# Kernel optimization log

Hardware: AMD Instinct MI355X
Metric: run time of the kernel (lower is better)

The kernel has to match this reference:

```python
import jax, jax.numpy as jnp
import numpy as np

N, E, F, ED, H, C, B = 50000, 200000, 768, 768, 256, 3, 4096


def setup_inputs() -> dict:
    key = jax.random.key(0)
    ks = jax.random.split(key, 20)
    s = 0.05  # init scale for params
    inp = {
        "x": jax.random.normal(ks[0], (N, F), jnp.float32),
        "edge_attr": jax.random.normal(ks[1], (E, ED), jnp.float32),
        # GATConv layer 1 (in=F, out=H, heads=1, edge_dim=ED)
        "W1": jax.random.normal(ks[2], (F, H), jnp.float32) * s,
        "as1": jax.random.normal(ks[3], (H,), jnp.float32) * s,
        "ad1": jax.random.normal(ks[4], (H,), jnp.float32) * s,
        "We1": jax.random.normal(ks[5], (ED, H), jnp.float32) * s,
        "ae1": jax.random.normal(ks[6], (H,), jnp.float32) * s,
        "b1": jnp.zeros((H,), jnp.float32),
        # GATConv layer 2 (in=H, out=H)
        "W2": jax.random.normal(ks[7], (H, H), jnp.float32) * s,
        "as2": jax.random.normal(ks[8], (H,), jnp.float32) * s,
        "ad2": jax.random.normal(ks[9], (H,), jnp.float32) * s,
        "We2": jax.random.normal(ks[10], (ED, H), jnp.float32) * s,
        "ae2": jax.random.normal(ks[11], (H,), jnp.float32) * s,
        "b2": jnp.zeros((H,), jnp.float32),
        # prediction head
        "Wp": jax.random.normal(ks[12], (H, C), jnp.float32) * s,
        "bp": jnp.zeros((C,), jnp.float32),
        "edge_index": jax.random.randint(ks[13], (2, E), 0, N, jnp.int32),
        "nodes": jax.random.randint(ks[14], (2, B), 0, N, jnp.int32),
    }
    return inp


def gat_conv(x, edge_attr, src, dst, W, a_src, a_dst, We, a_e, b, n):
    # GATConv, heads=1, edge_dim attention, add_self_loops=False
    xl = x @ W  # [n, H]
    alpha_src = (xl * a_src).sum(-1)  # [n]
    alpha_dst = (xl * a_dst).sum(-1)  # [n]
    alpha_edge = ((edge_attr @ We) * a_e).sum(-1)  # [E]
    alpha = alpha_src[src] + alpha_dst[dst] + alpha_edge  # [E]
    alpha = jax.nn.leaky_relu(alpha, 0.2)
    # scatter-softmax over incoming edges of each destination node
    m = jax.ops.segment_max(alpha, dst, num_segments=n)
    e = jnp.exp(alpha - m[dst])
    den = jax.ops.segment_sum(e, dst, num_segments=n)
    coef = e / den[dst]  # [E]
    out = jax.ops.segment_sum(coef[:, None] * xl[src], dst, num_segments=n)
    return out + b


def reference(x, edge_attr, W1, as1, ad1, We1, ae1, b1, W2, as2, ad2, We2, ae2, b2, Wp, bp, edge_index, nodes):
    src, dst = edge_index[0], edge_index[1]
    n = x.shape[0]
    h = jax.nn.relu(gat_conv(x, edge_attr, src, dst, W1, as1, ad1, We1, ae1, b1, n))
    titles = gat_conv(h, edge_attr, src, dst, W2, as2, ad2, We2, ae2, b2, n)
    c = titles[nodes[0]] * titles[nodes[1]]  # [B, H]
    return c @ Wp + bp
```

## Files before the change

### kernel.cpp

```cpp
#include <hip/hip_runtime.h>
#include <math.h>

#define HDIM 256
#define FDIM 768
#define BM 128
#define BK 32

typedef __attribute__((ext_vector_type(8))) short short8;
typedef __attribute__((ext_vector_type(4))) float f32x4;
typedef __attribute__((ext_vector_type(4))) unsigned short us4;

__device__ __forceinline__ unsigned short f2bf(float f) {
  unsigned int u = __float_as_uint(f);
  unsigned int r = (u + 0x7FFFu + ((u >> 16) & 1u)) >> 16;
  return (unsigned short)r;
}
__device__ __forceinline__ float bf2f(unsigned short b) {
  return __uint_as_float(((unsigned int)b) << 16);
}

__device__ __forceinline__ void gload_lds16(const void* g, void* l) {
  __builtin_amdgcn_global_load_lds(
      (const __attribute__((address_space(1))) void*)g,
      (__attribute__((address_space(3))) void*)l, 16, 0, 0);
}


__device__ __forceinline__ void transpose_tile(const float* __restrict__ W,
                                               unsigned short* __restrict__ Wt,
                                               int K, int tk, int tn,
                                               float (*sT)[65], int t) {
  int lane = t & 63, rg = t >> 6;
  #pragma unroll
  for (int i = 0; i < 16; ++i) {
    int r = rg * 16 + i;
    sT[lane][r] = W[(size_t)(tk * 64 + r) * HDIM + tn * 64 + lane];
  }
  __syncthreads();
  #pragma unroll
  for (int i = 0; i < 16; ++i) {
    int h = rg * 16 + i;
    Wt[(size_t)(tn * 64 + h) * K + tk * 64 + lane] = f2bf(sT[h][lane]);
  }
}

__global__ __launch_bounds__(256) void k_prep(
    const float* __restrict__ We1, const float* __restrict__ ae1,
    const float* __restrict__ We2, const float* __restrict__ ae2,
    float* __restrict__ v1, float* __restrict__ v2,
    const float* __restrict__ W1, unsigned short* __restrict__ W1t,
    const float* __restrict__ W2, unsigned short* __restrict__ W2t,
    const int* __restrict__ dstArr, int* __restrict__ cnt, int E) {
  __shared__ float sT[64][65];
  int bid = blockIdx.x;
  int t = threadIdx.x;
  if (bid < 384) {
    int row = bid * 4 + (t >> 6);
    int lane = t & 63;
    const float* W = (row < FDIM) ? We1 : We2;
    const float* a = (row < FDIM) ? ae1 : ae2;
    int r = (row < FDIM) ? row : row - FDIM;
    float4 w = *(const float4*)&W[(size_t)r * HDIM + lane * 4];
    float4 av = *(const float4*)&a[lane * 4];
    float p = w.x * av.x + w.y * av.y + w.z * av.z + w.w * av.w;
    #pragma unroll
    for (int off = 32; off; off >>= 1) p += __shfl_down(p, off, 64);
    if (lane == 0) ((row < FDIM) ? v1 : v2)[r] = p;
  } else if (bid < 432) {
    int tile = bid - 384;
    transpose_tile(W1, W1t, FDIM, tile % 12, tile / 12, sT, t);
  } else if (bid < 448) {
    int tile = bid - 432;
    transpose_tile(W2, W2t, HDIM, tile & 3, tile >> 2, sT, t);
  } else {
    int e = (bid - 448) * 256 + t;
    if (e < E) atomicAdd(&cnt[dstArr[e]], 1);
  }
}


__global__ __launch_bounds__(256) void k_scan_lb(const int* __restrict__ cnt,
                                                 int* __restrict__ offsets,
                                                 int* __restrict__ cursor,
                                                 int* __restrict__ bsums,
                                                 int* __restrict__ flags, int n) {
  __shared__ int s[256];
  __shared__ int r[256];
  const int b = blockIdx.x, t = threadIdx.x;
  int i = b * 256 + t;
  int v = (i < n) ? cnt[i] : 0;
  s[t] = v;
  __syncthreads();
  for (int off = 1; off < 256; off <<= 1) {
    int tv = (t >= off) ? s[t - off] : 0;
    __syncthreads();
    s[t] += tv;
    __syncthreads();
  }
  if (t == 255) {
    bsums[b] = s[255];
    __threadfence();
    __hip_atomic_store(&flags[b], 1, __ATOMIC_RELEASE, __HIP_MEMORY_SCOPE_AGENT);
  }
  int contrib = 0;
  if (t < b) {
    while (!__hip_atomic_load(&flags[t], __ATOMIC_ACQUIRE, __HIP_MEMORY_SCOPE_AGENT))
      __builtin_amdgcn_s_sleep(2);
    contrib = bsums[t];
  }
  r[t] = contrib;
  __syncthreads();
  #pragma unroll
  for (int off = 128; off; off >>= 1) {
    if (t < off) r[t] += r[t + off];
    __syncthreads();
  }
  int base = r[0];
  if (i < n) {
    int incl = base + s[t];
    offsets[i + 1] = incl;
    cursor[i] = incl - v;
    if (i == 0) offsets[0] = 0;
  }
}


template <bool AF32, bool COUTBF>
__device__ __forceinline__ void gemm_body(unsigned char* lds,
                                          const void* __restrict__ Ain,
                                          const unsigned short* __restrict__ Bt,
                                          void* __restrict__ Cout,
                                          float* __restrict__ sOut,
                                          float* __restrict__ dOut,
                                          const float* __restrict__ a_src,
                                          const float* __restrict__ a_dst,
                                          int M, int K, int tile) {
  unsigned char* As = lds;
  unsigned char* Bs = lds + 8192;
  float* partS = (float*)(lds + 24576);
  float* partD = (float*)(lds + 24576 + 2048);
  const int t = threadIdx.x;
  const int l = t & 63;
  const int w = t >> 6;
  const int wm = w >> 2, wn = w & 3;
  const int bm = tile * BM;

  f32x4 acc[4][4] = {};

  int rowA = bm + (t & 127);
  if (rowA >= M) rowA = M - 1;
  const int cA = t >> 7;
  int rowAr = bm + (t >> 2);
  if (rowAr >= M) rowAr = M - 1;
  const int kbAr = t & 3;
  const int sAr = kbAr * 2048 + (t >> 2) * 16;
  const int nB = t & 255;
  const int cB0 = t >> 8;
  const int cB1 = 2 + (t >> 8);

  int aAddr[4], bAddr[4];
  #pragma unroll
  for (int mt = 0; mt < 4; ++mt) {
    int m = wm * 64 + mt * 16 + (l & 15);
    aAddr[mt] = (l >> 4) * 2048 + m * 16;
  }
  #pragma unroll
  for (int nt = 0; nt < 4; ++nt) {
    int nn = wn * 64 + nt * 16 + (l & 15);
    bAddr[nt] = (l >> 4) * 4096 + nn * 16;
  }

  const int nsteps = K / BK;
  for (int ks = 0; ks < nsteps; ++ks) {
    const int k0 = ks * BK;
    __syncthreads();
    if (AF32) {
      const float* A = (const float*)Ain;
      const float* p = A + (size_t)rowAr * K + k0 + kbAr * 8;
      float4 f0 = *(const float4*)p;
      float4 f1 = *(const float4*)(p + 4);
      short8 hv;
      hv[0] = (short)f2bf(f0.x); hv[1] = (short)f2bf(f0.y);
      hv[2] = (short)f2bf(f0.z); hv[3] = (short)f2bf(f0.w);
      hv[4] = (short)f2bf(f1.x); hv[5] = (short)f2bf(f1.y);
      hv[6] = (short)f2bf(f1.z); hv[7] = (short)f2bf(f1.w);
      *(short8*)(As + sAr) = hv;
    } else {
      const unsigned short* A = (const unsigned short*)Ain;
      gload_lds16(A + (size_t)rowA * K + k0 + cA * 8, As + t * 16);
    }
    gload_lds16(Bt + (size_t)nB * K + k0 + cB0 * 8, Bs + t * 16);
    gload_lds16(Bt + (size_t)nB * K + k0 + cB1 * 8, Bs + 8192 + t * 16);
    __syncthreads();

    short8 af[4], bfr[4];
    #pragma unroll
    for (int mt = 0; mt < 4; ++mt) af[mt] = *(const short8*)(As + aAddr[mt]);
    #pragma unroll
    for (int nt = 0; nt < 4; ++nt) bfr[nt] = *(const short8*)(Bs + bAddr[nt]);
    #pragma unroll
    for (int mt = 0; mt < 4; ++mt)
      #pragma unroll
      for (int nt = 0; nt < 4; ++nt)
        acc[mt][nt] = __builtin_amdgcn_mfma_f32_16x16x32_bf16(af[mt], bfr[nt], acc[mt][nt], 0, 0, 0);
  }

  float asv[4], adv[4];
  #pragma unroll
  for (int nt = 0; nt < 4; ++nt) {
    int col = wn * 64 + nt * 16 + (l & 15);
    asv[nt] = a_src[col];
    adv[nt] = a_dst[col];
  }
  #pragma unroll
  for (int mt = 0; mt < 4; ++mt) {
    int rloc = wm * 64 + mt * 16 + ((l >> 4) << 2);
    #pragma unroll
    for (int r = 0; r < 4; ++r) {
      int row = bm + rloc + r;
      float ps = 0.f, pd = 0.f;
      #pragma unroll
      for (int nt = 0; nt < 4; ++nt) {
        float v = acc[mt][nt][r];
        if (row < M) {
          int col = wn * 64 + nt * 16 + (l & 15);
          if (COUTBF)
            ((unsigned short*)Cout)[(size_t)row * HDIM + col] = f2bf(v);
          else
            ((float*)Cout)[(size_t)row * HDIM + col] = v;
        }
        ps += v * asv[nt];
        pd += v * adv[nt];
      }
      #pragma unroll
      for (int off = 1; off < 16; off <<= 1) {
        ps += __shfl_xor(ps, off, 64);
        pd += __shfl_xor(pd, off, 64);
      }
      if ((l & 15) == 0) {
        partS[wn * 128 + rloc + r] = ps;
        partD[wn * 128 + rloc + r] = pd;
      }
    }
  }
  __syncthreads();
  if (t < 128) {
    int row = bm + t;
    if (row < M) {
      sOut[row] = partS[t] + partS[128 + t] + partS[256 + t] + partS[384 + t];
      dOut[row] = partD[t] + partD[128 + t] + partD[256 + t] + partD[384 + t];
    }
  }
}


__device__ __forceinline__ void edge_body(unsigned char* lds,
                                          const float* __restrict__ ea,
                                          const float* __restrict__ v1,
                                          const float* __restrict__ v2,
                                          float* __restrict__ o1,
                                          float* __restrict__ o2, int E, int ebid) {
  float* sv1 = (float*)lds;
  float* sv2 = (float*)(lds + 3072);
  for (int i = threadIdx.x; i < FDIM; i += 512) { sv1[i] = v1[i]; sv2[i] = v2[i]; }
  __syncthreads();
  int lane = threadIdx.x & 63;
  int base = ebid * 32 + (threadIdx.x >> 6) * 4;
  #pragma unroll
  for (int q = 0; q < 4; ++q) {
    int e = base + q;
    if (e >= E) break;
    const float* row = ea + (size_t)e * FDIM;
    float p1 = 0.f, p2 = 0.f;
    #pragma unroll
    for (int t = 0; t < 3; ++t) {
      int idx = t * 256 + lane * 4;
      float4 x = *(const float4*)&row[idx];
      float4 a = *(const float4*)&sv1[idx];
      float4 b = *(const float4*)&sv2[idx];
      p1 += x.x * a.x + x.y * a.y + x.z * a.z + x.w * a.w;
      p2 += x.x * b.x + x.y * b.y + x.z * b.z + x.w * b.w;
    }
    #pragma unroll
    for (int off = 32; off; off >>= 1) {
      p1 += __shfl_down(p1, off, 64);
      p2 += __shfl_down(p2, off, 64);
    }
    if (lane == 0) { o1[e] = p1; o2[e] = p2; }
  }
}


#define NSCAT 98

__global__ __launch_bounds__(512) void k_fat1(
    const float* __restrict__ x, const unsigned short* __restrict__ W1t,
    unsigned short* __restrict__ xl1b, float* __restrict__ sArr, float* __restrict__ dArr,
    const float* __restrict__ as1, const float* __restrict__ ad1, int M,
    const float* __restrict__ ea, const float* __restrict__ v1,
    const float* __restrict__ v2, float* __restrict__ ae1Arr,
    float* __restrict__ ae2Arr, int E, int nGemm,
    const int* __restrict__ dstArr, int* __restrict__ cursor,
    int* __restrict__ elist) {
  __shared__ unsigned char lds[28672];
  int bid = blockIdx.x;
  if (bid < nGemm) {
    gemm_body<true, true>(lds, x, W1t, xl1b, sArr, dArr, as1, ad1, M, FDIM, bid);
  } else if (bid < nGemm + NSCAT) {
    int sb = bid - nGemm;
    for (int e = sb * 512 + threadIdx.x; e < E; e += NSCAT * 512) {
      int p = atomicAdd(&cursor[dstArr[e]], 1);
      elist[p] = e;
    }
  } else {
    edge_body(lds, ea, v1, v2, ae1Arr, ae2Arr, E, bid - nGemm - NSCAT);
  }
}

__global__ __launch_bounds__(512) void k_gemm2(
    const unsigned short* __restrict__ hb, const unsigned short* __restrict__ W2t,
    unsigned short* __restrict__ xl2b, float* __restrict__ sArr, float* __restrict__ dArr,
    const float* __restrict__ as2, const float* __restrict__ ad2, int M) {
  __shared__ unsigned char lds[28672];
  gemm_body<false, true>(lds, hb, W2t, xl2b, sArr, dArr, as2, ad2, M, HDIM, blockIdx.x);
}


__device__ __forceinline__ void agg_node16(const unsigned short* __restrict__ xlb,
                                           const float* __restrict__ sArr,
                                           float dnode,
                                           const float* __restrict__ aeArr,
                                           const int* __restrict__ src,
                                           const int* __restrict__ elist,
                                           int beg, int end, int gl, float* a) {
  float run_m = -1e30f, run_den = 0.f;
  #pragma unroll
  for (int i = 0; i < 16; ++i) a[i] = 0.f;
  for (int c0 = beg; c0 < end; c0 += 16) {
    int j = c0 + gl;
    float al = -1e30f;
    int sj = 0;
    if (j < end) {
      int e = elist[j];
      sj = src[e];
      float aa = sArr[sj] + dnode + aeArr[e];
      al = (aa > 0.f) ? aa : 0.2f * aa;
    }
    float cm = al;
    #pragma unroll
    for (int off = 8; off; off >>= 1) cm = fmaxf(cm, __shfl_xor(cm, off, 16));
    float new_m = fmaxf(run_m, cm);
    float ev = (j < end) ? expf(al - new_m) : 0.f;
    float cs = ev;
    #pragma unroll
    for (int off = 8; off; off >>= 1) cs += __shfl_xor(cs, off, 16);
    float scale = expf(run_m - new_m);
    run_den = run_den * scale + cs;
    #pragma unroll
    for (int i = 0; i < 16; ++i) a[i] *= scale;
    int cdeg = end - c0;
    if (cdeg > 16) cdeg = 16;
    for (int q = 0; q < cdeg; ++q) {
      float wgt = __shfl(ev, q, 16);
      int sq = __shfl(sj, q, 16);
      const unsigned short* rp = xlb + (size_t)sq * HDIM + gl * 4;
      #pragma unroll
      for (int s = 0; s < 4; ++s) {
        us4 v = *(const us4*)(rp + s * 64);
        a[s * 4 + 0] += wgt * bf2f(v[0]);
        a[s * 4 + 1] += wgt * bf2f(v[1]);
        a[s * 4 + 2] += wgt * bf2f(v[2]);
        a[s * 4 + 3] += wgt * bf2f(v[3]);
      }
    }
    run_m = new_m;
  }
  float inv = (end > beg) ? 1.f / run_den : 0.f;
  #pragma unroll
  for (int i = 0; i < 16; ++i) a[i] *= inv;
}


__global__ __launch_bounds__(256) void k_aggregate1(const unsigned short* __restrict__ xlb,
                                                    const float* __restrict__ sArr,
                                                    const float* __restrict__ dArr,
                                                    const float* __restrict__ aeArr,
                                                    const int* __restrict__ src,
                                                    const int* __restrict__ offsets,
                                                    const int* __restrict__ elist,
                                                    const float* __restrict__ bias,
                                                    unsigned short* __restrict__ outb,
                                                    int n) {
  int grp = threadIdx.x >> 4;
  int gl = threadIdx.x & 15;
  int node = blockIdx.x * 16 + grp;
  if (node >= n) return;
  int beg = offsets[node], end = offsets[node + 1];
  float a[16];
  agg_node16(xlb, sArr, dArr[node], aeArr, src, elist, beg, end, gl, a);
  unsigned short* orow = outb + (size_t)node * HDIM + gl * 4;
  #pragma unroll
  for (int s = 0; s < 4; ++s) {
    float4 bv = *(const float4*)(bias + s * 64 + gl * 4);
    us4 ov;
    ov[0] = f2bf(fmaxf(a[s * 4 + 0] + bv.x, 0.f));
    ov[1] = f2bf(fmaxf(a[s * 4 + 1] + bv.y, 0.f));
    ov[2] = f2bf(fmaxf(a[s * 4 + 2] + bv.z, 0.f));
    ov[3] = f2bf(fmaxf(a[s * 4 + 3] + bv.w, 0.f));
    *(us4*)(orow + s * 64) = ov;
  }
}


__global__ __launch_bounds__(256) void k_agg2head(const unsigned short* __restrict__ xl2b,
                                                  const float* __restrict__ sArr,
                                                  const float* __restrict__ dArr,
                                                  const float* __restrict__ aeArr,
                                                  const int* __restrict__ src,
                                                  const int* __restrict__ offsets,
                                                  const int* __restrict__ elist,
                                                  const float* __restrict__ b2,
                                                  const int* __restrict__ nodes,
                                                  const float* __restrict__ Wp,
                                                  const float* __restrict__ bp,
                                                  float* __restrict__ out, int Bn) {
  __shared__ float tls[8][2][HDIM];
  int grp = threadIdx.x >> 4;
  int gl = threadIdx.x & 15;
  int pl = grp >> 1;
  int side = grp & 1;
  int b = blockIdx.x * 8 + pl;
  if (b < Bn) {
    int node = nodes[side * Bn + b];
    int beg = offsets[node], end = offsets[node + 1];
    float a[16];
    agg_node16(xl2b, sArr, dArr[node], aeArr, src, elist, beg, end, gl, a);
    #pragma unroll
    for (int s = 0; s < 4; ++s) {
      int h = s * 64 + gl * 4;
      float4 bv = *(const float4*)(b2 + h);
      float* dstp = &tls[pl][side][h];
      dstp[0] = a[s * 4 + 0] + bv.x;
      dstp[1] = a[s * 4 + 1] + bv.y;
      dstp[2] = a[s * 4 + 2] + bv.z;
      dstp[3] = a[s * 4 + 3] + bv.w;
    }
  }
  __syncthreads();
  if (b < Bn && side == 0) {
    float s0 = 0.f, s1 = 0.f, s2 = 0.f;
    #pragma unroll
    for (int s = 0; s < 4; ++s) {
      int h = s * 64 + gl * 4;
      float4 t0 = *(const float4*)&tls[pl][0][h];
      float4 t1 = *(const float4*)&tls[pl][1][h];
      float c0 = t0.x * t1.x, c1 = t0.y * t1.y, c2 = t0.z * t1.z, c3 = t0.w * t1.w;
      s0 += c0 * Wp[h * 3 + 0] + c1 * Wp[(h + 1) * 3 + 0] +
            c2 * Wp[(h + 2) * 3 + 0] + c3 * Wp[(h + 3) * 3 + 0];
      s1 += c0 * Wp[h * 3 + 1] + c1 * Wp[(h + 1) * 3 + 1] +
            c2 * Wp[(h + 2) * 3 + 1] + c3 * Wp[(h + 3) * 3 + 1];
      s2 += c0 * Wp[h * 3 + 2] + c1 * Wp[(h + 1) * 3 + 2] +
            c2 * Wp[(h + 2) * 3 + 2] + c3 * Wp[(h + 3) * 3 + 2];
    }
    #pragma unroll
    for (int off = 8; off; off >>= 1) {
      s0 += __shfl_down(s0, off, 16);
      s1 += __shfl_down(s1, off, 16);
      s2 += __shfl_down(s2, off, 16);
    }
    if (gl == 0) {
      out[b * 3 + 0] = s0 + bp[0];
      out[b * 3 + 1] = s1 + bp[1];
      out[b * 3 + 2] = s2 + bp[2];
    }
  }
}


extern "C" void kernel_launch(void* const* d_in, const int* in_sizes, int n_in,
                              void* d_out, int out_size, void* d_ws, size_t ws_size,
                              hipStream_t stream) {
  const float* x         = (const float*)d_in[0];
  const float* edge_attr = (const float*)d_in[1];
  const float* W1  = (const float*)d_in[2];
  const float* as1 = (const float*)d_in[3];
  const float* ad1 = (const float*)d_in[4];
  const float* We1 = (const float*)d_in[5];
  const float* ae1 = (const float*)d_in[6];
  const float* b1  = (const float*)d_in[7];
  const float* W2  = (const float*)d_in[8];
  const float* as2 = (const float*)d_in[9];
  const float* ad2 = (const float*)d_in[10];
  const float* We2 = (const float*)d_in[11];
  const float* ae2 = (const float*)d_in[12];
  const float* b2  = (const float*)d_in[13];
  const float* Wp  = (const float*)d_in[14];
  const float* bp  = (const float*)d_in[15];
  const int* edge_index = (const int*)d_in[16];
  const int* nodes      = (const int*)d_in[17];

  const int N  = in_sizes[0] / FDIM;
  const int E  = in_sizes[16] / 2;
  const int Bn = in_sizes[17] / 2;
  const int* srcArr = edge_index;
  const int* dstArr = edge_index + E;

  char* w = (char*)d_ws;
  auto carve = [&](size_t bytes) -> void* {
    void* p = (void*)w;
    w += (bytes + 255) & ~(size_t)255;
    return p;
  };
  unsigned short* xl1b   = (unsigned short*)carve(2 * (size_t)N * HDIM);
  unsigned short* hb     = (unsigned short*)carve(2 * (size_t)N * HDIM);
  unsigned short* W1t    = (unsigned short*)carve(2 * (size_t)FDIM * HDIM);
  unsigned short* W2t    = (unsigned short*)carve(2 * (size_t)HDIM * HDIM);
  float* ae1Arr = (float*)carve(sizeof(float) * E);
  float* ae2Arr = (float*)carve(sizeof(float) * E);
  float* sArr = (float*)carve(sizeof(float) * N);
  float* dArr = (float*)carve(sizeof(float) * N);
  float* v1 = (float*)carve(sizeof(float) * FDIM);
  float* v2 = (float*)carve(sizeof(float) * FDIM);
  int* cntflags = (int*)carve(sizeof(int) * (N + 256));
  int* offsets = (int*)carve(sizeof(int) * (N + 1));
  int* cursor  = (int*)carve(sizeof(int) * N);
  int* elist   = (int*)carve(sizeof(int) * E);
  int* bsums   = (int*)carve(sizeof(int) * 256);

  int* cnt = cntflags;
  int* flags = cntflags + N;

  const int nbScan = (N + 255) / 256;
  const int nbHist = (E + 255) / 256;
  const int nGemm = (N + BM - 1) / BM;
  const int nEdge = (E + 31) / 32;

  hipMemsetAsync(cntflags, 0, sizeof(int) * (N + 256), stream);
  k_prep<<<448 + nbHist, 256, 0, stream>>>(We1, ae1, We2, ae2, v1, v2,
                                           W1, W1t, W2, W2t, dstArr, cnt, E);
  k_scan_lb<<<nbScan, 256, 0, stream>>>(cnt, offsets, cursor, bsums, flags, N);

  k_fat1<<<nGemm + NSCAT + nEdge, 512, 0, stream>>>(
      x, W1t, xl1b, sArr, dArr, as1, ad1, N,
      edge_attr, v1, v2, ae1Arr, ae2Arr, E, nGemm, dstArr, cursor, elist);
  k_aggregate1<<<(N + 15) / 16, 256, 0, stream>>>(xl1b, sArr, dArr, ae1Arr, srcArr,
                                                  offsets, elist, b1, hb, N);
  k_gemm2<<<nGemm, 512, 0, stream>>>(hb, W2t, xl1b, sArr, dArr, as2, ad2, N);
  k_agg2head<<<(Bn + 7) / 8, 256, 0, stream>>>(xl1b, sArr, dArr, ae2Arr, srcArr,
                                               offsets, elist, b2, nodes, Wp, bp,
                                               (float*)d_out, Bn);
}
```

Measured before the change: 266.0 us.

## Specialize layer-2 GEMM with K=64 stages and double edges per block

Replaces the generic gemm_body call in k_gemm2 with a dedicated kernel. It stages 64-wide K slices of A and the full 256-column B tile in larger LDS buffers, so only four load/sync rounds are needed for K=256, and it fuses the bf16 output store with the per-row attention dot products. Separately, edge-attention blocks now process 64 edges instead of 32, halving block count and the per-block reload of the two projection vectors. The risks are lower occupancy from the larger LDS footprint (53 KB) and reduced parallelism in the edge phase.

```diff
diff --git a/kernel.cpp b/kernel.cpp
--- a/kernel.cpp
+++ b/kernel.cpp
@@ -265,9 +265,9 @@
   for (int i = threadIdx.x; i < FDIM; i += 512) { sv1[i] = v1[i]; sv2[i] = v2[i]; }
   __syncthreads();
   int lane = threadIdx.x & 63;
-  int base = ebid * 32 + (threadIdx.x >> 6) * 4;
-  #pragma unroll
-  for (int q = 0; q < 4; ++q) {
+  int base = ebid * 64 + (threadIdx.x >> 6) * 8;
+  #pragma unroll
+  for (int q = 0; q < 8; ++q) {
     int e = base + q;
     if (e >= E) break;
     const float* row = ea + (size_t)e * FDIM;
@@ -317,12 +317,117 @@
   }
 }
 
+
 __global__ __launch_bounds__(512) void k_gemm2(
-    const unsigned short* __restrict__ hb, const unsigned short* __restrict__ W2t,
-    unsigned short* __restrict__ xl2b, float* __restrict__ sArr, float* __restrict__ dArr,
-    const float* __restrict__ as2, const float* __restrict__ ad2, int M) {
-  __shared__ unsigned char lds[28672];
-  gemm_body<false, true>(lds, hb, W2t, xl2b, sArr, dArr, as2, ad2, M, HDIM, blockIdx.x);
+    const unsigned short* __restrict__ A, const unsigned short* __restrict__ Bt,
+    unsigned short* __restrict__ Cout, float* __restrict__ sOut,
+    float* __restrict__ dOut, const float* __restrict__ a_src,
+    const float* __restrict__ a_dst, int M) {
+  __shared__ unsigned char lds[53248];
+  unsigned char* As = lds;
+  unsigned char* Bs = lds + 16384;
+  float* partS = (float*)(lds + 49152);
+  float* partD = (float*)(lds + 49152 + 2048);
+  const int K = HDIM;
+  const int t = threadIdx.x;
+  const int l = t & 63;
+  const int w = t >> 6;
+  const int wm = w >> 2, wn = w & 3;
+  const int bm = blockIdx.x * BM;
+
+  f32x4 acc[4][4] = {};
+
+  int rowA = bm + (t & 127);
+  if (rowA >= M) rowA = M - 1;
+  const int cA0 = t >> 7;
+  const int cA1 = 4 + (t >> 7);
+  const int nB = t & 255;
+  const int cB[4] = {t >> 8, 2 + (t >> 8), 4 + (t >> 8), 6 + (t >> 8)};
+
+  int aAddr[2][4], bAddr[2][4];
+  #pragma unroll
+  for (int kk = 0; kk < 2; ++kk) {
+    #pragma unroll
+    for (int mt = 0; mt < 4; ++mt) {
+      int m = wm * 64 + mt * 16 + (l & 15);
+      aAddr[kk][mt] = (kk * 4 + (l >> 4)) * 2048 + m * 16;
+    }
+    #pragma unroll
+    for (int nt = 0; nt < 4; ++nt) {
+      int nn = wn * 64 + nt * 16 + (l & 15);
+      bAddr[kk][nt] = (kk * 4 + (l >> 4)) * 4096 + nn * 16;
+    }
+  }
+
+  #pragma unroll
+  for (int ks = 0; ks < 4; ++ks) {
+    const int k0 = ks * 64;
+    __syncthreads();
+    gload_lds16(A + (size_t)rowA * K + k0 + cA0 * 8, As + t * 16);
+    gload_lds16(A + (size_t)rowA * K + k0 + cA1 * 8, As + 8192 + t * 16);
+    #pragma unroll
+    for (int q = 0; q < 4; ++q)
+      gload_lds16(Bt + (size_t)nB * K + k0 + cB[q] * 8, Bs + q * 8192 + t * 16);
+    __syncthreads();
+
+    #pragma unroll
+    for (int kk = 0; kk < 2; ++kk) {
+      short8 af[4], bfr[4];
+      #pragma unroll
+      for (int mt = 0; mt < 4; ++mt) af[mt] = *(const short8*)(As + aAddr[kk][mt]);
+      #pragma unroll
+      for (int nt = 0; nt < 4; ++nt) bfr[nt] = *(const short8*)(Bs + bAddr[kk][nt]);
+      #pragma unroll
+      for (int mt = 0; mt < 4; ++mt)
+        #pragma unroll
+        for (int nt = 0; nt < 4; ++nt)
+          acc[mt][nt] = __builtin_amdgcn_mfma_f32_16x16x32_bf16(af[mt], bfr[nt], acc[mt][nt], 0, 0, 0);
+    }
+  }
+
+  float asv[4], adv[4];
+  #pragma unroll
+  for (int nt = 0; nt < 4; ++nt) {
+    int col = wn * 64 + nt * 16 + (l & 15);
+    asv[nt] = a_src[col];
+    adv[nt] = a_dst[col];
+  }
+  #pragma unroll
+  for (int mt = 0; mt < 4; ++mt) {
+    int rloc = wm * 64 + mt * 16 + ((l >> 4) << 2);
+    #pragma unroll
+    for (int r = 0; r < 4; ++r) {
+      int row = bm + rloc + r;
+      float ps = 0.f, pd = 0.f;
+      #pragma unroll
+      for (int nt = 0; nt < 4; ++nt) {
+        float v = acc[mt][nt][r];
+        if (row < M) {
+          int col = wn * 64 + nt * 16 + (l & 15);
+          Cout[(size_t)row * HDIM + col] = f2bf(v);
+        }
+        ps += v * asv[nt];
+        pd += v * adv[nt];
+      }
+      #pragma unroll
+      for (int off = 1; off < 16; off <<= 1) {
+        ps += __shfl_xor(ps, off, 64);
+        pd += __shfl_xor(pd, off, 64);
+      }
+      if ((l & 15) == 0) {
+        partS[wn * 128 + rloc + r] = ps;
+        partD[wn * 128 + rloc + r] = pd;
+      }
+    }
+  }
+  __syncthreads();
+  if (t < 128) {
+    int row = bm + t;
+    if (row < M) {
+      sOut[row] = partS[t] + partS[128 + t] + partS[256 + t] + partS[384 + t];
+      dOut[row] = partD[t] + partD[128 + t] + partD[256 + t] + partD[384 + t];
+    }
+  }
 }
 
 
@@ -533,7 +638,7 @@
   const int nbScan = (N + 255) / 256;
   const int nbHist = (E + 255) / 256;
   const int nGemm = (N + BM - 1) / BM;
-  const int nEdge = (E + 31) / 32;
+  const int nEdge = (E + 63) / 64;
 
   hipMemsetAsync(cntflags, 0, sizeof(int) * (N + 256), stream);
   k_prep<<<448 + nbHist, 256, 0, stream>>>(We1, ae1, We2, ae2, v1, v2,
```

Result: no change. 268.7 us (+1.0%).
